# Kernel tuning notes

Measured on AMD Instinct MI355X. Metric: run time of the kernel, lower is better.

Reference implementation:

```python
import jax, jax.numpy as jnp
import numpy as np

EPS = 1e-5
ROPE_BASE = 10000.0

def _rms_norm(x, alpha):
    # var = eps + mean(x^2) (eps added to mean, matching _rms_norm)
    var = EPS + jnp.mean(x * x, axis=-1, keepdims=True)
    return x * (alpha * jax.lax.rsqrt(var))

def _rope(x, pos):
    # x: [B,H,T,D], pos: [T] absolute positions; interleaved pair rotation
    D = x.shape[-1]
    half = D // 2
    inv_freq = ROPE_BASE ** (-jnp.arange(half, dtype=x.dtype) / half)
    ang = pos.astype(x.dtype)[:, None] * inv_freq[None, :]          # [T,half]
    cos, sin = jnp.cos(ang), jnp.sin(ang)
    x1, x2 = x[..., ::2], x[..., 1::2]
    y1 = x1 * cos - x2 * sin
    y2 = x1 * sin + x2 * cos
    return jnp.stack([y1, y2], axis=-1).reshape(x.shape)

def setup_inputs() -> dict:
    key = jax.random.key(0)
    ks = jax.random.split(key, 9)
    B, T, C = 8, 256, 2048
    H, Dh, CAP, FF = 16, 128, 2048, 8192
    s = 0.02
    return {
        "x": jax.random.normal(ks[0], (B, T, C), jnp.float32),
        "kcache": jax.random.normal(ks[1], (B, H, CAP, Dh), jnp.float32) * s,
        "vcache": jax.random.normal(ks[2], (B, H, CAP, Dh), jnp.float32) * s,
        "in_proj_w": jax.random.normal(ks[3], (3 * C, C), jnp.float32) * s,
        "out_proj_w": jax.random.normal(ks[4], (C, C), jnp.float32) * s,
        "norm1_a": jnp.ones((C,), jnp.float32),
        "norm2_a": jnp.ones((C,), jnp.float32),
        "w1": jax.random.normal(ks[5], (FF, C), jnp.float32) * s,
        "w2": jax.random.normal(ks[6], (C, FF), jnp.float32) * s,
        "offset": 1024,
    }

def reference(x, kcache, vcache, in_proj_w, out_proj_w, norm1_a, norm2_a, w1, w2, offset):
    B, T, C = x.shape
    H = 16
    Dh = C // H
    CAP = kcache.shape[2]
    scale = 1.0 / np.sqrt(Dh)

    # ---- self-attention branch ----
    xn = _rms_norm(x, norm1_a)
    qkv = jnp.einsum('btc,oc->bto', xn, in_proj_w)                  # [B,T,3C]
    q, k, v = jnp.split(qkv, 3, axis=-1)
    def heads(t):  # [B,T,C] -> [B,H,T,Dh]
        return t.reshape(B, T, H, Dh).transpose(0, 2, 1, 3)
    q, k, v = heads(q), heads(k), heads(v)

    t_abs = offset + jnp.arange(T)                                   # absolute positions
    q = _rope(q, t_abs)
    k = _rope(k, t_abs)

    # ---- ring KV cache write: idx = (offset + t) % capacity ----
    widx = (offset + jnp.arange(T)) % CAP                            # [T]
    kcache = kcache.at[:, :, widx, :].set(k)
    vcache = vcache.at[:, :, widx, :].set(v)

    # ---- recover absolute positions of cache slots (RingKVCache.complete) ----
    idx = jnp.arange(CAP)
    last = offset + T - 1
    end_index = last % CAP
    delta = idx - end_index
    pos = jnp.where(delta <= 0, last + delta, last + delta - CAP)    # [CAP]
    invalid = idx >= (offset + T)
    pos = jnp.where(invalid, -1, pos)

    # ---- causal + context masked attention over full cache ----
    qpos = offset + jnp.arange(T)                                    # [T]
    d = qpos[:, None] - pos[None, :]                                 # [T,CAP]
    mask = (pos[None, :] >= 0) & (d >= 0) & (d < CAP)
    scores = jnp.einsum('bhtd,bhsd->bhts', q, kcache) * scale        # [B,H,T,CAP]
    scores = jnp.where(mask[None, None], scores, jnp.float32(-1e9))
    attn = jax.nn.softmax(scores, axis=-1)
    o = jnp.einsum('bhts,bhsd->bhtd', attn, vcache)                  # [B,H,T,Dh]
    o = o.transpose(0, 2, 1, 3).reshape(B, T, C)
    x = x + jnp.einsum('btc,oc->bto', o, out_proj_w)

    # ---- MLP branch ----
    h = _rms_norm(x, norm2_a)
    h = jax.nn.gelu(jnp.einsum('btc,fc->btf', h, w1), approximate=False)
    x = x + jnp.einsum('btf,cf->btc', h, w2)
    return x
```

## Files before the change

kernel.cpp:

```cpp
#include <hip/hip_runtime.h>
#include <math.h>


typedef __bf16 bf16_t;
typedef __bf16 bf16x8 __attribute__((ext_vector_type(8)));
typedef float  f32x4  __attribute__((ext_vector_type(4)));

#define MFMA(a, b, c) __builtin_amdgcn_mfma_f32_16x16x32_bf16((a), (b), (c), 0, 0, 0)

static __device__ __forceinline__ bf16x8 cvt8(const float* __restrict__ src) {
    f32x4 f0 = *(const f32x4*)src;
    f32x4 f1 = *(const f32x4*)(src + 4);
    bf16x8 v;
    v[0] = (bf16_t)f0[0]; v[1] = (bf16_t)f0[1]; v[2] = (bf16_t)f0[2]; v[3] = (bf16_t)f0[3];
    v[4] = (bf16_t)f1[0]; v[5] = (bf16_t)f1[1]; v[6] = (bf16_t)f1[2]; v[7] = (bf16_t)f1[3];
    return v;
}

static __device__ __forceinline__ void gload16(const bf16_t* g, bf16_t* lds) {
    __builtin_amdgcn_global_load_lds(
        (const __attribute__((address_space(1))) void*)g,
        (__attribute__((address_space(3))) void*)lds, 16, 0, 0);
}

__global__ __launch_bounds__(256)
void cvt_rows_kernel(const float* __restrict__ src, bf16_t* __restrict__ dst,
                     int cols, int src_stride)
{
    const int row = blockIdx.x;
    const float* s = src + (size_t)row * src_stride;
    bf16_t* d = dst + (size_t)row * cols;
    for (int c = threadIdx.x * 8; c < cols; c += blockDim.x * 8)
        *(bf16x8*)&d[c] = cvt8(&s[c]);
}

__global__ __launch_bounds__(256)
void rmsnorm_kernel(const float* __restrict__ x, const float* __restrict__ alpha,
                    bf16_t* __restrict__ out)
{
    const int C = 2048;
    const int row = blockIdx.x;
    const int tid = threadIdx.x;
    const float* xr = x + (size_t)row * C;
    f32x4 a0 = *(const f32x4*)&xr[tid * 8];
    f32x4 a1 = *(const f32x4*)&xr[tid * 8 + 4];
    float ss = a0[0]*a0[0] + a0[1]*a0[1] + a0[2]*a0[2] + a0[3]*a0[3]
             + a1[0]*a1[0] + a1[1]*a1[1] + a1[2]*a1[2] + a1[3]*a1[3];
    #pragma unroll
    for (int d = 32; d >= 1; d >>= 1) ss += __shfl_xor(ss, d);
    __shared__ float red[4];
    const int lane = tid & 63, wid = tid >> 6;
    if (lane == 0) red[wid] = ss;
    __syncthreads();
    const float tot = red[0] + red[1] + red[2] + red[3];
    const float rs = rsqrtf(1e-5f + tot * (1.0f / C));
    f32x4 l0 = *(const f32x4*)&alpha[tid * 8];
    f32x4 l1 = *(const f32x4*)&alpha[tid * 8 + 4];
    bf16x8 o8;
    o8[0] = (bf16_t)(a0[0] * l0[0] * rs); o8[1] = (bf16_t)(a0[1] * l0[1] * rs);
    o8[2] = (bf16_t)(a0[2] * l0[2] * rs); o8[3] = (bf16_t)(a0[3] * l0[3] * rs);
    o8[4] = (bf16_t)(a1[0] * l1[0] * rs); o8[5] = (bf16_t)(a1[1] * l1[1] * rs);
    o8[6] = (bf16_t)(a1[2] * l1[2] * rs); o8[7] = (bf16_t)(a1[3] * l1[3] * rs);
    *(bf16x8*)&out[(size_t)row * C + tid * 8] = o8;
}

template<int EPI, int NSPLIT>
__global__ __launch_bounds__(256)
void gemm_bb(const bf16_t* __restrict__ A, const bf16_t* __restrict__ B,
             float* Cf, bf16_t* Cb, const float* __restrict__ res,
             int M, int N, int K, int lda, int ldb)
{
    __shared__ bf16_t As[128 * 64];
    __shared__ bf16_t Bs[128 * 64];
    if constexpr (NSPLIT > 1) {
        A  += (size_t)blockIdx.z * K;
        B  += (size_t)blockIdx.z * K;
        Cb += (size_t)blockIdx.z * (size_t)M * N;
    }
    const int gx = gridDim.x;
    const int nwg = gx * gridDim.y;
    int bid = blockIdx.y * gx + blockIdx.x;
    bid = (bid & 7) * (nwg >> 3) + (bid >> 3);
    const int n0 = (bid % gx) * 128;
    const int m0 = (bid / gx) * 128;

    const int tid = threadIdx.x;
    const int lane = tid & 63, wid = tid >> 6;
    const int wr = wid >> 1, wc = wid & 1;
    const int lr = lane & 15, lg = lane >> 4;
    const int srow = lane >> 3;
    const int scol = (lane & 7) * 8;
    f32x4 acc[4][4] = {};

    for (int kt = 0; kt < K; kt += 64) {
        __syncthreads();
        #pragma unroll
        for (int it = 0; it < 4; ++it) {
            const int r = wid * 32 + it * 8;
            gload16(&A[(size_t)(m0 + r + srow) * lda + kt + scol], &As[r * 64]);
            gload16(&B[(size_t)(n0 + r + srow) * ldb + kt + scol], &Bs[r * 64]);
        }
        __syncthreads();
        #pragma unroll
        for (int kk = 0; kk < 2; ++kk) {
            bf16x8 af[4], bfr[4];
            #pragma unroll
            for (int m = 0; m < 4; ++m)
                af[m] = *(const bf16x8*)&As[(wr * 64 + m * 16 + lr) * 64 + kk * 32 + lg * 8];
            #pragma unroll
            for (int n = 0; n < 4; ++n)
                bfr[n] = *(const bf16x8*)&Bs[(wc * 64 + n * 16 + lr) * 64 + kk * 32 + lg * 8];
            #pragma unroll
            for (int m = 0; m < 4; ++m)
                #pragma unroll
                for (int n = 0; n < 4; ++n)
                    acc[m][n] = MFMA(af[m], bfr[n], acc[m][n]);
        }
    }
    #pragma unroll
    for (int m = 0; m < 4; ++m) {
        #pragma unroll
        for (int n = 0; n < 4; ++n) {
            const int gmb = m0 + wr * 64 + m * 16 + lg * 4;
            const int gn  = n0 + wc * 64 + n * 16 + lr;
            #pragma unroll
            for (int r = 0; r < 4; ++r) {
                const size_t off = (size_t)(gmb + r) * N + gn;
                const float v = acc[m][n][r];
                if (EPI == 0)      Cf[off] = v;
                else if (EPI == 1) Cf[off] = res[off] + v;
                else if (EPI == 2) Cb[off] = (bf16_t)(0.5f * v * (1.0f + erff(v * 0.70710678118654752f)));
                else               Cb[off] = (bf16_t)v;
            }
        }
    }
}

template<int Z>
__global__ __launch_bounds__(256)
void reduce_sk_kernel(const bf16_t* __restrict__ p, const float* __restrict__ res,
                      float* __restrict__ out, int n)
{
    for (int i = (blockIdx.x * 256 + threadIdx.x) * 8; i < n; i += gridDim.x * 256 * 8) {
        f32x4 r0 = *(const f32x4*)&res[i];
        f32x4 r1 = *(const f32x4*)&res[i + 4];
        #pragma unroll
        for (int z = 0; z < Z; ++z) {
            bf16x8 v = *(const bf16x8*)&p[(size_t)z * n + i];
            r0[0] += (float)v[0]; r0[1] += (float)v[1]; r0[2] += (float)v[2]; r0[3] += (float)v[3];
            r1[0] += (float)v[4]; r1[1] += (float)v[5]; r1[2] += (float)v[6]; r1[7 - 7] += 0.0f;
            r1[3] += (float)v[7];
        }
        *(f32x4*)&out[i] = r0;
        *(f32x4*)&out[i + 4] = r1;
    }
}

__global__ __launch_bounds__(256)
void rope_split_kernel(const bf16_t* __restrict__ qkv,
                       bf16_t* __restrict__ q, bf16_t* __restrict__ kn,
                       bf16_t* __restrict__ vn, const int* __restrict__ offp)
{
    const int m = blockIdx.x;
    const int b = m >> 8, t = m & 255;
    const int tid = threadIdx.x;
    const int c = tid * 8;
    const int h = c >> 7, d0 = c & 127;
    const int pos = offp[0] + t;
    bf16x8 qv = *(const bf16x8*)&qkv[(size_t)m * 6144 + c];
    bf16x8 kv = *(const bf16x8*)&qkv[(size_t)m * 6144 + 2048 + c];
    bf16x8 vv = *(const bf16x8*)&qkv[(size_t)m * 6144 + 4096 + c];
    bf16x8 qo, ko;
    #pragma unroll
    for (int p = 0; p < 4; ++p) {
        const int i = (d0 >> 1) + p;
        const float ang = (float)pos * __expf(-(float)i * 0.14391156861538527f);
        const float sn = sinf(ang), cs = cosf(ang);
        const float q1 = (float)qv[2 * p], q2 = (float)qv[2 * p + 1];
        const float k1 = (float)kv[2 * p], k2 = (float)kv[2 * p + 1];
        qo[2 * p]     = (bf16_t)(q1 * cs - q2 * sn);
        qo[2 * p + 1] = (bf16_t)(q1 * sn + q2 * cs);
        ko[2 * p]     = (bf16_t)(k1 * cs - k2 * sn);
        ko[2 * p + 1] = (bf16_t)(k1 * sn + k2 * cs);
    }
    const size_t oi = (((size_t)(b * 16 + h) * 256) + t) * 128 + d0;
    *(bf16x8*)&q[oi]  = qo;
    *(bf16x8*)&kn[oi] = ko;
    *(bf16x8*)&vn[oi] = vv;
}

__global__ __launch_bounds__(256)
void attn_kernel(const bf16_t* __restrict__ qh, const bf16_t* __restrict__ kn,
                 const bf16_t* __restrict__ vn, const float* __restrict__ kcache,
                 const float* __restrict__ vcache, bf16_t* __restrict__ outp,
                 const int* __restrict__ offp)
{
    const int T = 256, Dh = 128, CAP = 2048, H = 16;
    const float scale = 0.08838834764831845f;
    __shared__ bf16_t Ks[64][136];
    __shared__ bf16_t VtL[128 * 64];
    __shared__ bf16_t Pl[4][16][72];
    const int bh = blockIdx.x;
    const int t0 = blockIdx.y * 64;
    const int b = bh >> 4, h = bh & 15;
    const int offset = offp[0];
    const int Stot = offset + T;
    const int tid = threadIdx.x, lane = tid & 63, wid = tid >> 6;
    const int lr = lane & 15, lg = lane >> 4;

    bf16x8 qf[4];
    {
        const bf16_t* qbase = qh + ((size_t)bh * T + t0 + wid * 16) * Dh;
        #pragma unroll
        for (int ks = 0; ks < 4; ++ks)
            qf[ks] = *(const bf16x8*)&qbase[lr * Dh + ks * 32 + lg * 8];
    }
    f32x4 accO[8] = {};
    float mrun[4], lrun[4];
    #pragma unroll
    for (int r = 0; r < 4; ++r) { mrun[r] = -3e38f; lrun[r] = 0.0f; }

    int smax = offset + t0 + 64; if (smax > Stot) smax = Stot;
    const int nch = (smax + 63) >> 6;

    for (int ch = 0; ch < nch; ++ch) {
        const int s0 = ch * 64;
        __syncthreads();
        #pragma unroll
        for (int it = 0; it < 4; ++it) {
            const int idx = tid + it * 256;
            const int r = idx >> 4, c8 = idx & 15;
            const int s = s0 + r;
            bf16x8 kv8, vv8;
            if (s < offset) {
                const size_t base = (((size_t)b * H + h) * CAP + s) * Dh + c8 * 8;
                kv8 = cvt8(&kcache[base]);
                vv8 = cvt8(&vcache[base]);
            } else if (s < Stot) {
                const size_t base = ((size_t)bh * T + (s - offset)) * Dh + c8 * 8;
                kv8 = *(const bf16x8*)&kn[base];
                vv8 = *(const bf16x8*)&vn[base];
            } else {
                #pragma unroll
                for (int j = 0; j < 8; ++j) { kv8[j] = (bf16_t)0.0f; vv8[j] = (bf16_t)0.0f; }
            }
            *(bf16x8*)&Ks[r][c8 * 8] = kv8;
            #pragma unroll
            for (int j = 0; j < 8; ++j)
                VtL[(c8 * 8 + j) * 64 + ((((r >> 3) ^ j ^ (c8 & 7))) << 3) + (r & 7)] = vv8[j];
        }
        __syncthreads();

        f32x4 sc[4] = {};
        #pragma unroll
        for (int ks = 0; ks < 4; ++ks) {
            bf16x8 kf[4];
            #pragma unroll
            for (int n = 0; n < 4; ++n)
                kf[n] = *(const bf16x8*)&Ks[n * 16 + lr][ks * 32 + lg * 8];
            #pragma unroll
            for (int n = 0; n < 4; ++n)
                sc[n] = MFMA(qf[ks], kf[n], sc[n]);
        }

        #pragma unroll
        for (int r = 0; r < 4; ++r) {
            const int qpos = offset + t0 + wid * 16 + lg * 4 + r;
            float mx = -3e38f;
            #pragma unroll
            for (int n = 0; n < 4; ++n) {
                const int sabs = s0 + n * 16 + lr;
                float v = sc[n][r] * scale;
                v = (sabs <= qpos && sabs < Stot) ? v : -1e30f;
                sc[n][r] = v;
                mx = fmaxf(mx, v);
            }
            #pragma unroll
            for (int d = 8; d >= 1; d >>= 1) mx = fmaxf(mx, __shfl_xor(mx, d));
            const float mo = mrun[r];
            const float mn2 = fmaxf(mo, mx);
            const float al = __expf(mo - mn2);
            mrun[r] = mn2;
            lrun[r] *= al;
            #pragma unroll
            for (int df = 0; df < 8; ++df) accO[df][r] *= al;
            float rsum = 0.0f;
            #pragma unroll
            for (int n = 0; n < 4; ++n) {
                const float p = __expf(sc[n][r] - mn2);
                sc[n][r] = p;
                rsum += p;
            }
            #pragma unroll
            for (int d = 8; d >= 1; d >>= 1) rsum += __shfl_xor(rsum, d);
            lrun[r] += rsum;
            #pragma unroll
            for (int n = 0; n < 4; ++n)
                Pl[wid][lg * 4 + r][n * 16 + lr] = (bf16_t)sc[n][r];
        }
        asm volatile("s_waitcnt lgkmcnt(0)" ::: "memory");
        __builtin_amdgcn_sched_barrier(0);

        #pragma unroll
        for (int ks2 = 0; ks2 < 2; ++ks2) {
            const bf16x8 pa = *(const bf16x8*)&Pl[wid][lr][ks2 * 32 + lg * 8];
            #pragma unroll
            for (int df = 0; df < 8; ++df) {
                const int d = df * 16 + lr;
                const bf16x8 vb8 = *(const bf16x8*)
                    &VtL[d * 64 + (((ks2 * 4 + lg) ^ (d & 7) ^ ((d >> 3) & 7)) << 3)];
                accO[df] = MFMA(pa, vb8, accO[df]);
            }
        }
    }

    float rinv[4];
    #pragma unroll
    for (int r = 0; r < 4; ++r) rinv[r] = 1.0f / lrun[r];
    #pragma unroll
    for (int df = 0; df < 8; ++df) {
        #pragma unroll
        for (int r = 0; r < 4; ++r) {
            const int t = t0 + wid * 16 + lg * 4 + r;
            outp[((size_t)b * 256 + t) * 2048 + h * 128 + df * 16 + lr] =
                (bf16_t)(accO[df][r] * rinv[r]);
        }
    }
}

extern "C" void kernel_launch(void* const* d_in, const int* in_sizes, int n_in,
                              void* d_out, int out_size, void* d_ws, size_t ws_size,
                              hipStream_t stream)
{
    const float* x    = (const float*)d_in[0];
    const float* kc   = (const float*)d_in[1];
    const float* vc   = (const float*)d_in[2];
    const float* wqkv = (const float*)d_in[3];
    const float* wo   = (const float*)d_in[4];
    const float* a1   = (const float*)d_in[5];
    const float* a2   = (const float*)d_in[6];
    const float* w1   = (const float*)d_in[7];
    const float* w2   = (const float*)d_in[8];
    const int*   offp = (const int*)d_in[9];
    float* out = (float*)d_out;

    char* ws = (char*)d_ws;
    bf16_t* xn     = (bf16_t*)(ws + 0);
    bf16_t* wqkv_b = (bf16_t*)(ws + (8ull  << 20));
    bf16_t* qkv    = (bf16_t*)(ws + (32ull << 20));
    bf16_t* q      = (bf16_t*)(ws + (8ull  << 20));
    bf16_t* kn     = (bf16_t*)(ws + (16ull << 20));
    bf16_t* vn     = (bf16_t*)(ws + (24ull << 20));
    bf16_t* wo_b   = (bf16_t*)(ws + (32ull << 20));
    bf16_t* o      = (bf16_t*)(ws + (40ull << 20));
    bf16_t* oprt   = (bf16_t*)(ws + (48ull << 20));
    bf16_t* hbuf   = (bf16_t*)(ws + 0);
    const bool bigws = ws_size >= (137ull << 20);

    rmsnorm_kernel<<<2048, 256, 0, stream>>>(x, a1, xn);
    cvt_rows_kernel<<<6144, 256, 0, stream>>>(wqkv, wqkv_b, 2048, 2048);
    gemm_bb<3, 1><<<dim3(48, 16), 256, 0, stream>>>(xn, wqkv_b, nullptr, qkv, nullptr,
                                                    2048, 6144, 2048, 2048, 2048);
    rope_split_kernel<<<2048, 256, 0, stream>>>(qkv, q, kn, vn, offp);
    cvt_rows_kernel<<<2048, 256, 0, stream>>>(wo, wo_b, 2048, 2048);
    attn_kernel<<<dim3(128, 4), 256, 0, stream>>>(q, kn, vn, kc, vc, o, offp);
    gemm_bb<3, 2><<<dim3(16, 16, 2), 256, 0, stream>>>(o, wo_b, nullptr, oprt, nullptr,
                                                       2048, 2048, 1024, 2048, 2048);
    reduce_sk_kernel<2><<<2048, 256, 0, stream>>>(oprt, x, out, 2048 * 2048);
    rmsnorm_kernel<<<2048, 256, 0, stream>>>(out, a2, hbuf);

    if (bigws) {
        bf16_t* w1b = (bf16_t*)(ws + (8ull   << 20));
        bf16_t* g   = (bf16_t*)(ws + (40ull  << 20));
        bf16_t* w2b = (bf16_t*)(ws + (72ull  << 20));
        bf16_t* prt = (bf16_t*)(ws + (104ull << 20));
        cvt_rows_kernel<<<8192, 256, 0, stream>>>(w1, w1b, 2048, 2048);
        gemm_bb<2, 1><<<dim3(64, 16), 256, 0, stream>>>(hbuf, w1b, nullptr, g, nullptr,
                                                        2048, 8192, 2048, 2048, 2048);
        cvt_rows_kernel<<<2048, 256, 0, stream>>>(w2, w2b, 8192, 8192);
        gemm_bb<3, 4><<<dim3(16, 16, 4), 256, 0, stream>>>(g, w2b, nullptr, prt, nullptr,
                                                           2048, 2048, 2048, 8192, 8192);
        reduce_sk_kernel<4><<<2048, 256, 0, stream>>>(prt, out, out, 2048 * 2048);
    } else {
        bf16_t* w1b = (bf16_t*)(ws + (8ull  << 20));
        bf16_t* g_h = (bf16_t*)(ws + (24ull << 20));
        bf16_t* w2b = (bf16_t*)(ws + (40ull << 20));
        bf16_t* prt = (bf16_t*)(ws + (8ull  << 20));
        for (int hh = 0; hh < 2; ++hh) {
            cvt_rows_kernel<<<4096, 256, 0, stream>>>(w1 + (size_t)hh * 4096 * 2048, w1b, 2048, 2048);
            gemm_bb<2, 1><<<dim3(32, 16), 256, 0, stream>>>(hbuf, w1b, nullptr, g_h, nullptr,
                                                            2048, 4096, 2048, 2048, 2048);
            cvt_rows_kernel<<<2048, 256, 0, stream>>>(w2 + (size_t)hh * 4096, w2b, 4096, 8192);
            gemm_bb<3, 2><<<dim3(16, 16, 2), 256, 0, stream>>>(g_h, w2b, nullptr, prt, nullptr,
                                                               2048, 2048, 2048, 4096, 4096);
            reduce_sk_kernel<2><<<2048, 256, 0, stream>>>(prt, out, out, 2048 * 2048);
        }
    }
}
```

Before: 517.6 us.

## Double-buffer LDS tiles in bf16 GEMM to overlap global loads with MFMA

The GEMM kernel now keeps two LDS buffers for the A and B tiles. It issues the async global-to-LDS loads for the next K tile before running the MFMAs on the current one, and uses a single barrier per iteration instead of two. It also raises wave priority around the MFMA block with s_setprio. This is meant to hide global load latency behind compute, at the cost of doubling LDS use per block, which may reduce occupancy. A no-op statement in the split-K reduction is also removed.

```diff
diff --git a/kernel.cpp b/kernel.cpp
--- a/kernel.cpp
+++ b/kernel.cpp
@@ -70,8 +70,8 @@
              float* Cf, bf16_t* Cb, const float* __restrict__ res,
              int M, int N, int K, int lda, int ldb)
 {
-    __shared__ bf16_t As[128 * 64];
-    __shared__ bf16_t Bs[128 * 64];
+    __shared__ bf16_t As[2][128 * 64];
+    __shared__ bf16_t Bs[2][128 * 64];
     if constexpr (NSPLIT > 1) {
         A  += (size_t)blockIdx.z * K;
         B  += (size_t)blockIdx.z * K;
@@ -92,31 +92,45 @@
     const int scol = (lane & 7) * 8;
     f32x4 acc[4][4] = {};
 
-    for (int kt = 0; kt < K; kt += 64) {
-        __syncthreads();
-        #pragma unroll
-        for (int it = 0; it < 4; ++it) {
-            const int r = wid * 32 + it * 8;
-            gload16(&A[(size_t)(m0 + r + srow) * lda + kt + scol], &As[r * 64]);
-            gload16(&B[(size_t)(n0 + r + srow) * ldb + kt + scol], &Bs[r * 64]);
-        }
-        __syncthreads();
+    const int nt = K >> 6;
+    const bf16_t* Ab = A + (size_t)m0 * lda;
+    const bf16_t* Bb = B + (size_t)n0 * ldb;
+
+    #define STAGE(bufi, kt)                                                          \
+        _Pragma("unroll")                                                            \
+        for (int it = 0; it < 4; ++it) {                                             \
+            const int r = wid * 32 + it * 8;                                         \
+            gload16(&Ab[(size_t)(r + srow) * lda + (kt) + scol], &As[bufi][r * 64]); \
+            gload16(&Bb[(size_t)(r + srow) * ldb + (kt) + scol], &Bs[bufi][r * 64]); \
+        }
+
+    STAGE(0, 0);
+    __syncthreads();
+    int cur = 0;
+    for (int t = 0; t < nt; ++t) {
+        if (t + 1 < nt) STAGE(cur ^ 1, (t + 1) << 6);
+        __builtin_amdgcn_s_setprio(1);
         #pragma unroll
         for (int kk = 0; kk < 2; ++kk) {
             bf16x8 af[4], bfr[4];
             #pragma unroll
             for (int m = 0; m < 4; ++m)
-                af[m] = *(const bf16x8*)&As[(wr * 64 + m * 16 + lr) * 64 + kk * 32 + lg * 8];
+                af[m] = *(const bf16x8*)&As[cur][(wr * 64 + m * 16 + lr) * 64 + kk * 32 + lg * 8];
             #pragma unroll
             for (int n = 0; n < 4; ++n)
-                bfr[n] = *(const bf16x8*)&Bs[(wc * 64 + n * 16 + lr) * 64 + kk * 32 + lg * 8];
+                bfr[n] = *(const bf16x8*)&Bs[cur][(wc * 64 + n * 16 + lr) * 64 + kk * 32 + lg * 8];
             #pragma unroll
             for (int m = 0; m < 4; ++m)
                 #pragma unroll
                 for (int n = 0; n < 4; ++n)
                     acc[m][n] = MFMA(af[m], bfr[n], acc[m][n]);
         }
-    }
+        __builtin_amdgcn_s_setprio(0);
+        __syncthreads();
+        cur ^= 1;
+    }
+    #undef STAGE
+
     #pragma unroll
     for (int m = 0; m < 4; ++m) {
         #pragma unroll
@@ -148,8 +162,7 @@
         for (int z = 0; z < Z; ++z) {
             bf16x8 v = *(const bf16x8*)&p[(size_t)z * n + i];
             r0[0] += (float)v[0]; r0[1] += (float)v[1]; r0[2] += (float)v[2]; r0[3] += (float)v[3];
-            r1[0] += (float)v[4]; r1[1] += (float)v[5]; r1[2] += (float)v[6]; r1[7 - 7] += 0.0f;
-            r1[3] += (float)v[7];
+            r1[0] += (float)v[4]; r1[1] += (float)v[5]; r1[2] += (float)v[6]; r1[3] += (float)v[7];
         }
         *(f32x4*)&out[i] = r0;
         *(f32x4*)&out[i + 4] = r1;
```

Measured after the change: 519.9 us. About the same (+0.4%).
